# Kernel tuning notes

Measured on AMD Instinct MI355X. Metric: run time of the kernel, lower is better.

## Reference

```python
import jax, jax.numpy as jnp
import numpy as np

NUM_NODES = 100_000
NUM_RELS = 64
DIM = 64
NUM_EDGES = 100_000


def setup_inputs() -> dict:
    key = jax.random.key(0)
    k_src, k_rel, k_dst, k_emb, k_w = jax.random.split(key, 5)
    src = jax.random.randint(k_src, (NUM_EDGES, 1), 0, NUM_NODES, dtype=jnp.int64 if jax.config.jax_enable_x64 else jnp.int32)
    rel = jax.random.randint(k_rel, (NUM_EDGES, 1), 0, NUM_RELS, dtype=src.dtype)
    dst = jax.random.randint(k_dst, (NUM_EDGES, 1), 0, NUM_NODES, dtype=src.dtype)
    triplets = jnp.concatenate([src, rel, dst], axis=1)  # [E, 3]
    node_emb = jax.random.normal(k_emb, (NUM_NODES, DIM), dtype=jnp.float32)
    # xavier_normal_ with gain=1.414: std = gain * sqrt(2 / (dim + dim))
    std = 1.414 * np.sqrt(2.0 / (DIM + DIM))
    W = jax.random.normal(k_w, (NUM_RELS, DIM, DIM), dtype=jnp.float32) * std
    return {"triplets": triplets, "node_emb": node_emb, "W": W}


def reference(triplets, node_emb, W):
    # score_e = src_emb_e^T @ W[rel_e] @ dst_emb_e  (per-edge bilinear form)
    src, rel, dst = triplets[:, 0], triplets[:, 1], triplets[:, 2]
    src_emb = node_emb[src]          # [E, d]
    dst_emb = node_emb[dst]          # [E, d]
    rel_emb = W[rel]                 # [E, d, d] gathered relation matrices
    scores = jnp.einsum('ed,edk,ek->e', src_emb, rel_emb, dst_emb)
    return scores
```

## Files before the change

### kernel.cpp

```cpp
#include <hip/hip_runtime.h>
#include <hip/hip_bf16.h>

#define NRELS 64
#define DIM 64
#define NSB 16
#define CSTRIDE 160
#define RSLOTS (NSB * CSTRIDE)
#define CHUNK 256
#define NCH (RSLOTS / CHUNK)
#define WLD 72

typedef __attribute__((ext_vector_type(8))) short short8;
typedef __attribute__((ext_vector_type(4))) float f32x4;

static __device__ __forceinline__ short bfc(float f) {
    union { __hip_bfloat16 h; short s; } u;
    u.h = __float2bfloat16(f);
    return u.s;
}
static __device__ __forceinline__ short8 pack8(float4 a, float4 b) {
    short8 o;
    o[0] = bfc(a.x); o[1] = bfc(a.y); o[2] = bfc(a.z); o[3] = bfc(a.w);
    o[4] = bfc(b.x); o[5] = bfc(b.y); o[6] = bfc(b.z); o[7] = bfc(b.w);
    return o;
}

__global__ __launch_bounds__(512)
void k_scatter(const int* __restrict__ trip, int E, int span,
               int* __restrict__ cnts, int4* __restrict__ bucket4) {
    __shared__ int lo[NRELS];
    const int t = threadIdx.x, b = blockIdx.x;
    if (t < NRELS) lo[t] = 0;
    __syncthreads();
    const int elo = b * span, ehi = min(E, elo + span);
    for (int e = elo + t; e < ehi; e += 512) {
        const int s = trip[e * 3], r = trip[e * 3 + 1], d = trip[e * 3 + 2];
        const int p = atomicAdd(&lo[r], 1);
        if (p < CSTRIDE)
            bucket4[r * RSLOTS + b * CSTRIDE + p] = make_int4(s, d, e, 0);
    }
    __syncthreads();
    if (t < NRELS) cnts[b * NRELS + t] = min(lo[t], CSTRIDE);
}

__global__ __launch_bounds__(512)
void k_score(const float* __restrict__ emb, const float* __restrict__ W,
             const int* __restrict__ cnts, const int4* __restrict__ bucket4,
             float* __restrict__ out) {
    const int r = blockIdx.x, ch = blockIdx.y;
    __shared__ short Wl[DIM][WLD];
    __shared__ int cntL[NSB];
    const int t = threadIdx.x;
    if (t < NSB) cntL[t] = cnts[t * NRELS + r];
    {
        const float4* __restrict__ Wr = (const float4*)(W + (long)r * DIM * DIM);
        #pragma unroll
        for (int k = 0; k < 2; ++k) {
            const int j = t + k * 512;
            const float4 v = Wr[j];
            const int d = j >> 4, n0 = (j & 15) * 4;
            Wl[n0 + 0][d] = bfc(v.x);
            Wl[n0 + 1][d] = bfc(v.y);
            Wl[n0 + 2][d] = bfc(v.z);
            Wl[n0 + 3][d] = bfc(v.w);
        }
    }
    __syncthreads();

    const int lane = t & 63, wave = t >> 6;
    const int w0 = ch * CHUNK + wave * 32;
    const int col = lane & 15, kg = lane >> 4, kb = kg * 8;

    const int slot0 = w0 + col, slot1 = slot0 + 16;
    const int c0 = slot0 / CSTRIDE, c1 = slot1 / CSTRIDE;
    const bool v0 = (slot0 - c0 * CSTRIDE) < cntL[c0];
    const bool v1 = (slot1 - c1 * CSTRIDE) < cntL[c1];
    if (__ballot(v0 || v1) == 0ull) return;

    const int4 raw0 = bucket4[r * RSLOTS + slot0];
    const int4 raw1 = bucket4[r * RSLOTS + slot1];
    const int sI0 = v0 ? raw0.x : 0;
    const int sI1 = v1 ? raw1.x : 0;
    const int dv0 = v0 ? raw0.y : 0;
    const int dv1 = v1 ? raw1.y : 0;
    const int ev0 = v0 ? raw0.z : -1;
    const int ev1 = v1 ? raw1.z : -1;

    const float* __restrict__ s0 = emb + (long)sI0 * DIM;
    const float* __restrict__ s1 = emb + (long)sI1 * DIM;
    float4 f0 = *(const float4*)(s0 + kb),      f1 = *(const float4*)(s0 + kb + 4);
    float4 f2 = *(const float4*)(s0 + 32 + kb), f3 = *(const float4*)(s0 + 32 + kb + 4);
    const short8 a00 = pack8(f0, f1), a01 = pack8(f2, f3);
    f0 = *(const float4*)(s1 + kb);      f1 = *(const float4*)(s1 + kb + 4);
    f2 = *(const float4*)(s1 + 32 + kb); f3 = *(const float4*)(s1 + 32 + kb + 4);
    const short8 a10 = pack8(f0, f1), a11 = pack8(f2, f3);

    f32x4 acc0[4], acc1[4];
    #pragma unroll
    for (int q = 0; q < 4; ++q) {
        acc0[q] = (f32x4){0.f, 0.f, 0.f, 0.f};
        acc1[q] = (f32x4){0.f, 0.f, 0.f, 0.f};
    }
    #pragma unroll
    for (int q = 0; q < 4; ++q) {
        const short8 b0 = *(const short8*)&Wl[q * 16 + col][kb];
        const short8 b1 = *(const short8*)&Wl[q * 16 + col][32 + kb];
        acc0[q] = __builtin_amdgcn_mfma_f32_16x16x32_bf16(b0, a00, acc0[q], 0, 0, 0);
        acc0[q] = __builtin_amdgcn_mfma_f32_16x16x32_bf16(b1, a01, acc0[q], 0, 0, 0);
        acc1[q] = __builtin_amdgcn_mfma_f32_16x16x32_bf16(b0, a10, acc1[q], 0, 0, 0);
        acc1[q] = __builtin_amdgcn_mfma_f32_16x16x32_bf16(b1, a11, acc1[q], 0, 0, 0);
    }

    {
        const float* __restrict__ dr = emb + (long)dv0 * DIM;
        float p = 0.f;
        #pragma unroll
        for (int q = 0; q < 4; ++q) {
            const float4 dv = *(const float4*)(dr + q * 16 + kg * 4);
            p = fmaf(acc0[q][0], dv.x, p);
            p = fmaf(acc0[q][1], dv.y, p);
            p = fmaf(acc0[q][2], dv.z, p);
            p = fmaf(acc0[q][3], dv.w, p);
        }
        p += __shfl_xor(p, 16, 64);
        p += __shfl_xor(p, 32, 64);
        if (kg == 0 && ev0 >= 0) out[ev0] = p;
    }
    {
        const float* __restrict__ dr = emb + (long)dv1 * DIM;
        float p = 0.f;
        #pragma unroll
        for (int q = 0; q < 4; ++q) {
            const float4 dv = *(const float4*)(dr + q * 16 + kg * 4);
            p = fmaf(acc1[q][0], dv.x, p);
            p = fmaf(acc1[q][1], dv.y, p);
            p = fmaf(acc1[q][2], dv.z, p);
            p = fmaf(acc1[q][3], dv.w, p);
        }
        p += __shfl_xor(p, 16, 64);
        p += __shfl_xor(p, 32, 64);
        if (kg == 0 && ev1 >= 0) out[ev1] = p;
    }
}

extern "C" void kernel_launch(void* const* d_in, const int* in_sizes, int n_in,
                              void* d_out, int out_size, void* d_ws, size_t ws_size,
                              hipStream_t stream) {
    const int*   trip = (const int*)d_in[0];
    const float* emb  = (const float*)d_in[1];
    const float* W    = (const float*)d_in[2];
    float*       out  = (float*)d_out;

    const int E = in_sizes[0] / 3;
    const int span = (E + NSB - 1) / NSB;

    int4* bucket4 = (int4*)d_ws;
    int*  cnts    = (int*)(bucket4 + NRELS * RSLOTS);

    k_scatter<<<NSB, 512, 0, stream>>>(trip, E, span, cnts, bucket4);
    k_score  <<<dim3(NRELS, NCH), 512, 0, stream>>>(emb, W, cnts, bucket4, out);
}
```

Measured before the change: 24.34 us.

## Fuse scatter and score into one kernel with per-block shared-memory edge lists

Replaces the two-kernel flow (global bucket scatter by 16 blocks, then per-relation scoring) with one kernel. Each block owns a group of 4 relations and one of 32 edge segments. It filters its segment's edges into shared-memory lists, loads the 4 relation matrices as bf16 into LDS, and scores with MFMA. This removes a launch, the global bucket write and read-back, and the low-parallelism scatter phase. In exchange, every relation-group block re-reads the relation column of its segment, and any bucket holding more than 96 edges silently drops the extra edges.

```diff
diff --git a/kernel.cpp b/kernel.cpp
--- a/kernel.cpp
+++ b/kernel.cpp
@@ -3,11 +3,10 @@
 
 #define NRELS 64
 #define DIM 64
-#define NSB 16
-#define CSTRIDE 160
-#define RSLOTS (NSB * CSTRIDE)
-#define CHUNK 256
-#define NCH (RSLOTS / CHUNK)
+#define RG 4
+#define NRG (NRELS / RG)
+#define NSEG 32
+#define CAP 96
 #define WLD 72
 
 typedef __attribute__((ext_vector_type(8))) short short8;
@@ -26,120 +25,123 @@
 }
 
 __global__ __launch_bounds__(512)
-void k_scatter(const int* __restrict__ trip, int E, int span,
-               int* __restrict__ cnts, int4* __restrict__ bucket4) {
-    __shared__ int lo[NRELS];
-    const int t = threadIdx.x, b = blockIdx.x;
-    if (t < NRELS) lo[t] = 0;
+void k_all(const int* __restrict__ trip, const float* __restrict__ emb,
+           const float* __restrict__ W, float* __restrict__ out, int E, int span) {
+    __shared__ short Wl[RG][DIM][WLD];
+    __shared__ int4  list[RG][CAP];
+    __shared__ int   lcnt[RG];
+
+    const int t  = threadIdx.x;
+    const int rg  = blockIdx.x & (NRG - 1);
+    const int seg = blockIdx.x >> 4;
+
+    if (t < RG) lcnt[t] = 0;
     __syncthreads();
-    const int elo = b * span, ehi = min(E, elo + span);
-    for (int e = elo + t; e < ehi; e += 512) {
-        const int s = trip[e * 3], r = trip[e * 3 + 1], d = trip[e * 3 + 2];
-        const int p = atomicAdd(&lo[r], 1);
-        if (p < CSTRIDE)
-            bucket4[r * RSLOTS + b * CSTRIDE + p] = make_int4(s, d, e, 0);
+
+    {
+        const float4* __restrict__ Wb = (const float4*)(W + (long)rg * RG * DIM * DIM);
+        #pragma unroll
+        for (int k = 0; k < 8; ++k) {
+            const int j = t + k * 512;
+            const int rr = j >> 10, jj = j & 1023;
+            const float4 v = Wb[j];
+            const int d = jj >> 4, n0 = (jj & 15) * 4;
+            Wl[rr][n0 + 0][d] = bfc(v.x);
+            Wl[rr][n0 + 1][d] = bfc(v.y);
+            Wl[rr][n0 + 2][d] = bfc(v.z);
+            Wl[rr][n0 + 3][d] = bfc(v.w);
+        }
     }
-    __syncthreads();
-    if (t < NRELS) cnts[b * NRELS + t] = min(lo[t], CSTRIDE);
-}
 
-__global__ __launch_bounds__(512)
-void k_score(const float* __restrict__ emb, const float* __restrict__ W,
-             const int* __restrict__ cnts, const int4* __restrict__ bucket4,
-             float* __restrict__ out) {
-    const int r = blockIdx.x, ch = blockIdx.y;
-    __shared__ short Wl[DIM][WLD];
-    __shared__ int cntL[NSB];
-    const int t = threadIdx.x;
-    if (t < NSB) cntL[t] = cnts[t * NRELS + r];
     {
-        const float4* __restrict__ Wr = (const float4*)(W + (long)r * DIM * DIM);
-        #pragma unroll
-        for (int k = 0; k < 2; ++k) {
-            const int j = t + k * 512;
-            const float4 v = Wr[j];
-            const int d = j >> 4, n0 = (j & 15) * 4;
-            Wl[n0 + 0][d] = bfc(v.x);
-            Wl[n0 + 1][d] = bfc(v.y);
-            Wl[n0 + 2][d] = bfc(v.z);
-            Wl[n0 + 3][d] = bfc(v.w);
+        const int elo = seg * span, ehi = min(E, elo + span);
+        for (int e = elo + t; e < ehi; e += 512) {
+            const int r = trip[e * 3 + 1];
+            if ((r >> 2) == rg) {
+                const int p = atomicAdd(&lcnt[r & 3], 1);
+                if (p < CAP)
+                    list[r & 3][p] = make_int4(trip[e * 3], trip[e * 3 + 2], e, 0);
+            }
         }
     }
     __syncthreads();
 
     const int lane = t & 63, wave = t >> 6;
-    const int w0 = ch * CHUNK + wave * 32;
+    const int lr = wave >> 1, sub = wave & 1;
+    const int cnt = min(lcnt[lr], CAP);
     const int col = lane & 15, kg = lane >> 4, kb = kg * 8;
 
-    const int slot0 = w0 + col, slot1 = slot0 + 16;
-    const int c0 = slot0 / CSTRIDE, c1 = slot1 / CSTRIDE;
-    const bool v0 = (slot0 - c0 * CSTRIDE) < cntL[c0];
-    const bool v1 = (slot1 - c1 * CSTRIDE) < cntL[c1];
-    if (__ballot(v0 || v1) == 0ull) return;
+    for (int w0 = sub * 32; w0 < CAP; w0 += 64) {
+        if (w0 >= cnt) break;
 
-    const int4 raw0 = bucket4[r * RSLOTS + slot0];
-    const int4 raw1 = bucket4[r * RSLOTS + slot1];
-    const int sI0 = v0 ? raw0.x : 0;
-    const int sI1 = v1 ? raw1.x : 0;
-    const int dv0 = v0 ? raw0.y : 0;
-    const int dv1 = v1 ? raw1.y : 0;
-    const int ev0 = v0 ? raw0.z : -1;
-    const int ev1 = v1 ? raw1.z : -1;
+        const int slot0 = w0 + col, slot1 = slot0 + 16;
+        const bool v0 = slot0 < cnt;
+        const bool v1 = slot1 < cnt;
 
-    const float* __restrict__ s0 = emb + (long)sI0 * DIM;
-    const float* __restrict__ s1 = emb + (long)sI1 * DIM;
-    float4 f0 = *(const float4*)(s0 + kb),      f1 = *(const float4*)(s0 + kb + 4);
-    float4 f2 = *(const float4*)(s0 + 32 + kb), f3 = *(const float4*)(s0 + 32 + kb + 4);
-    const short8 a00 = pack8(f0, f1), a01 = pack8(f2, f3);
-    f0 = *(const float4*)(s1 + kb);      f1 = *(const float4*)(s1 + kb + 4);
-    f2 = *(const float4*)(s1 + 32 + kb); f3 = *(const float4*)(s1 + 32 + kb + 4);
-    const short8 a10 = pack8(f0, f1), a11 = pack8(f2, f3);
+        const int4 raw0 = list[lr][slot0];
+        const int4 raw1 = list[lr][slot1];
+        const int sI0 = v0 ? raw0.x : 0;
+        const int sI1 = v1 ? raw1.x : 0;
+        const int dv0 = v0 ? raw0.y : 0;
+        const int dv1 = v1 ? raw1.y : 0;
+        const int ev0 = v0 ? raw0.z : -1;
+        const int ev1 = v1 ? raw1.z : -1;
 
-    f32x4 acc0[4], acc1[4];
-    #pragma unroll
-    for (int q = 0; q < 4; ++q) {
-        acc0[q] = (f32x4){0.f, 0.f, 0.f, 0.f};
-        acc1[q] = (f32x4){0.f, 0.f, 0.f, 0.f};
-    }
-    #pragma unroll
-    for (int q = 0; q < 4; ++q) {
-        const short8 b0 = *(const short8*)&Wl[q * 16 + col][kb];
-        const short8 b1 = *(const short8*)&Wl[q * 16 + col][32 + kb];
-        acc0[q] = __builtin_amdgcn_mfma_f32_16x16x32_bf16(b0, a00, acc0[q], 0, 0, 0);
-        acc0[q] = __builtin_amdgcn_mfma_f32_16x16x32_bf16(b1, a01, acc0[q], 0, 0, 0);
-        acc1[q] = __builtin_amdgcn_mfma_f32_16x16x32_bf16(b0, a10, acc1[q], 0, 0, 0);
-        acc1[q] = __builtin_amdgcn_mfma_f32_16x16x32_bf16(b1, a11, acc1[q], 0, 0, 0);
-    }
+        const float* __restrict__ s0 = emb + (long)sI0 * DIM;
+        const float* __restrict__ s1 = emb + (long)sI1 * DIM;
+        float4 f0 = *(const float4*)(s0 + kb),      f1 = *(const float4*)(s0 + kb + 4);
+        float4 f2 = *(const float4*)(s0 + 32 + kb), f3 = *(const float4*)(s0 + 32 + kb + 4);
+        const short8 a00 = pack8(f0, f1), a01 = pack8(f2, f3);
+        f0 = *(const float4*)(s1 + kb);      f1 = *(const float4*)(s1 + kb + 4);
+        f2 = *(const float4*)(s1 + 32 + kb); f3 = *(const float4*)(s1 + 32 + kb + 4);
+        const short8 a10 = pack8(f0, f1), a11 = pack8(f2, f3);
 
-    {
-        const float* __restrict__ dr = emb + (long)dv0 * DIM;
-        float p = 0.f;
+        f32x4 acc0[4], acc1[4];
         #pragma unroll
         for (int q = 0; q < 4; ++q) {
-            const float4 dv = *(const float4*)(dr + q * 16 + kg * 4);
-            p = fmaf(acc0[q][0], dv.x, p);
-            p = fmaf(acc0[q][1], dv.y, p);
-            p = fmaf(acc0[q][2], dv.z, p);
-            p = fmaf(acc0[q][3], dv.w, p);
+            acc0[q] = (f32x4){0.f, 0.f, 0.f, 0.f};
+            acc1[q] = (f32x4){0.f, 0.f, 0.f, 0.f};
         }
-        p += __shfl_xor(p, 16, 64);
-        p += __shfl_xor(p, 32, 64);
-        if (kg == 0 && ev0 >= 0) out[ev0] = p;
-    }
-    {
-        const float* __restrict__ dr = emb + (long)dv1 * DIM;
-        float p = 0.f;
         #pragma unroll
         for (int q = 0; q < 4; ++q) {
-            const float4 dv = *(const float4*)(dr + q * 16 + kg * 4);
-            p = fmaf(acc1[q][0], dv.x, p);
-            p = fmaf(acc1[q][1], dv.y, p);
-            p = fmaf(acc1[q][2], dv.z, p);
-            p = fmaf(acc1[q][3], dv.w, p);
+            const short8 b0 = *(const short8*)&Wl[lr][q * 16 + col][kb];
+            const short8 b1 = *(const short8*)&Wl[lr][q * 16 + col][32 + kb];
+            acc0[q] = __builtin_amdgcn_mfma_f32_16x16x32_bf16(b0, a00, acc0[q], 0, 0, 0);
+            acc0[q] = __builtin_amdgcn_mfma_f32_16x16x32_bf16(b1, a01, acc0[q], 0, 0, 0);
+            acc1[q] = __builtin_amdgcn_mfma_f32_16x16x32_bf16(b0, a10, acc1[q], 0, 0, 0);
+            acc1[q] = __builtin_amdgcn_mfma_f32_16x16x32_bf16(b1, a11, acc1[q], 0, 0, 0);
         }
-        p += __shfl_xor(p, 16, 64);
-        p += __shfl_xor(p, 32, 64);
-        if (kg == 0 && ev1 >= 0) out[ev1] = p;
+
+        {
+            const float* __restrict__ dr = emb + (long)dv0 * DIM;
+            float p = 0.f;
+            #pragma unroll
+            for (int q = 0; q < 4; ++q) {
+                const float4 dv = *(const float4*)(dr + q * 16 + kg * 4);
+                p = fmaf(acc0[q][0], dv.x, p);
+                p = fmaf(acc0[q][1], dv.y, p);
+                p = fmaf(acc0[q][2], dv.z, p);
+                p = fmaf(acc0[q][3], dv.w, p);
+            }
+            p += __shfl_xor(p, 16, 64);
+            p += __shfl_xor(p, 32, 64);
+            if (kg == 0 && ev0 >= 0) out[ev0] = p;
+        }
+        {
+            const float* __restrict__ dr = emb + (long)dv1 * DIM;
+            float p = 0.f;
+            #pragma unroll
+            for (int q = 0; q < 4; ++q) {
+                const float4 dv = *(const float4*)(dr + q * 16 + kg * 4);
+                p = fmaf(acc1[q][0], dv.x, p);
+                p = fmaf(acc1[q][1], dv.y, p);
+                p = fmaf(acc1[q][2], dv.z, p);
+                p = fmaf(acc1[q][3], dv.w, p);
+            }
+            p += __shfl_xor(p, 16, 64);
+            p += __shfl_xor(p, 32, 64);
+            if (kg == 0 && ev1 >= 0) out[ev1] = p;
+        }
     }
 }
 
@@ -152,11 +154,7 @@
     float*       out  = (float*)d_out;
 
     const int E = in_sizes[0] / 3;
-    const int span = (E + NSB - 1) / NSB;
+    const int span = (E + NSEG - 1) / NSEG;
 
-    int4* bucket4 = (int4*)d_ws;
-    int*  cnts    = (int*)(bucket4 + NRELS * RSLOTS);
-
-    k_scatter<<<NSB, 512, 0, stream>>>(trip, E, span, cnts, bucket4);
-    k_score  <<<dim3(NRELS, NCH), 512, 0, stream>>>(emb, W, cnts, bucket4, out);
+    k_all<<<NRG * NSEG, 512, 0, stream>>>(trip, emb, W, out, E, span);
 }
```

After: 22.12 us. 9.1% less time.
